# Kernel optimization log

Hardware: AMD Instinct MI355X
Metric: run time of the kernel (lower is better)

## Reference

```python
import jax, jax.numpy as jnp
import numpy as np

HIDDEN = 2048
NUM_HEADS = 16
HEAD_DIM = 128
BLOCK_SIZE = 64
NUM_ACTIVE_BLOCKS = 4  # diagonal pattern -> bandwidth = 2 blocks each side
NEG_INF = -1e30  # stand-in for -inf that is safe under softmax in fp32


def _block_diagonal_additive_mask(seq_len: int) -> jnp.ndarray:
    """Token-level additive mask [S, S]; 0 where block |bi-bj|<=bandwidth, -inf else."""
    bandwidth = NUM_ACTIVE_BLOCKS // 2
    bid = jnp.arange(seq_len) // BLOCK_SIZE  # [S]
    active = jnp.abs(bid[:, None] - bid[None, :]) <= bandwidth  # [S, S] bool
    return jnp.where(active, 0.0, NEG_INF).astype(jnp.float32)


def setup_inputs() -> dict:
    key = jax.random.key(0)
    k0, k1, k2, k3, k4 = jax.random.split(key, 5)
    B, S = 2, 2048
    scale = 1.0 / np.sqrt(HIDDEN)
    return {
        "hidden_states": jax.random.normal(k0, (B, S, HIDDEN), dtype=jnp.float32),
        "Wq": jax.random.normal(k1, (HIDDEN, NUM_HEADS * HEAD_DIM), dtype=jnp.float32) * scale,
        "Wk": jax.random.normal(k2, (HIDDEN, NUM_HEADS * HEAD_DIM), dtype=jnp.float32) * scale,
        "Wv": jax.random.normal(k3, (HIDDEN, NUM_HEADS * HEAD_DIM), dtype=jnp.float32) * scale,
        "Wo": jax.random.normal(k4, (NUM_HEADS * HEAD_DIM, HIDDEN), dtype=jnp.float32) * scale,
    }


def reference(hidden_states, Wq, Wk, Wv, Wo):
    B, S, _ = hidden_states.shape
    scaling = HEAD_DIM ** -0.5

    # projections -> [B, H, S, D]
    def split_heads(x):
        return x.reshape(B, S, NUM_HEADS, HEAD_DIM).transpose(0, 2, 1, 3)

    q = split_heads(hidden_states @ Wq)
    k = split_heads(hidden_states @ Wk)
    v = split_heads(hidden_states @ Wv)

    mask = _block_diagonal_additive_mask(S)  # [S, S]

    # scores [B, H, S, S]
    scores = jnp.einsum("bhsd,bhtd->bhst", q, k) * scaling + mask[None, None]
    attn = jax.nn.softmax(scores.astype(jnp.float32), axis=-1).astype(q.dtype)

    out = jnp.einsum("bhst,bhtd->bhsd", attn, v)  # [B, H, S, D]
    out = out.transpose(0, 2, 1, 3).reshape(B, S, NUM_HEADS * HEAD_DIM)
    return out @ Wo
```

## Files before the change

### kernel.cpp

```cpp
#include <hip/hip_runtime.h>

typedef __attribute__((ext_vector_type(4))) float f32x4;
typedef __attribute__((ext_vector_type(16))) float f32x16;
typedef __attribute__((ext_vector_type(8))) _Float16 f16x8;
typedef __attribute__((ext_vector_type(4))) _Float16 f16x4;

__device__ __forceinline__ void gload_lds16(const void* g, void* l) {
  __builtin_amdgcn_global_load_lds((__attribute__((address_space(1))) void*)(g),
                                   (__attribute__((address_space(3))) void*)(l), 16, 0, 0);
}

#define SB0() __builtin_amdgcn_sched_barrier(0)
#define WAITV6() asm volatile("s_waitcnt vmcnt(6)" ::: "memory")
#define WAITV0() asm volatile("s_waitcnt vmcnt(0)" ::: "memory")

__global__ __launch_bounds__(256) void prep(const float* __restrict__ Hs,
                                            const float* __restrict__ W0, const float* __restrict__ W1,
                                            const float* __restrict__ W2, const float* __restrict__ W3,
                                            _Float16* __restrict__ Hb, _Float16* __restrict__ Wt) {
  __shared__ _Float16 tile[64][65];
  const int bid = blockIdx.x, tid = threadIdx.x;
  if (bid < 8192) {
    int i = (bid * 256 + tid) * 4;
    float4 v = *(const float4*)(Hs + i);
    f16x4 o = { (_Float16)v.x, (_Float16)v.y, (_Float16)v.z, (_Float16)v.w };
    *(f16x4*)(Hb + i) = o;
    return;
  }
  const int t = bid - 8192;
  const int z = t >> 10, k0 = ((t >> 5) & 31) * 64, n0 = (t & 31) * 64;
  const float* W = z == 0 ? W0 : z == 1 ? W1 : z == 2 ? W2 : W3;
  _Float16* Wo_ = Wt + (size_t)z * (2048u * 2048u);
  #pragma unroll
  for (int p = 0; p < 4; ++p) {
    int o = p * 256 + tid, r = o >> 4, c = o & 15;
    float4 v = *(const float4*)(W + (size_t)(k0 + r) * 2048 + n0 + c * 4);
    tile[r][c * 4 + 0] = (_Float16)v.x;
    tile[r][c * 4 + 1] = (_Float16)v.y;
    tile[r][c * 4 + 2] = (_Float16)v.z;
    tile[r][c * 4 + 3] = (_Float16)v.w;
  }
  __syncthreads();
  #pragma unroll
  for (int p = 0; p < 2; ++p) {
    int o = p * 256 + tid, nl = o >> 3, c = o & 7;
    f16x8 u;
    #pragma unroll
    for (int i = 0; i < 8; ++i) u[i] = tile[c * 8 + i][nl];
    *(f16x8*)(Wo_ + (size_t)(n0 + nl) * 2048 + k0 + c * 8) = u;
  }
}

template <int SM, int SN, typename OutT>
__device__ __forceinline__ void gemm_tile(const _Float16* __restrict__ A,
                                          const _Float16* __restrict__ Bt,
                                          OutT* __restrict__ C,
                                          int K, int N, int m0, int n0, _Float16* S) {
  _Float16* As = S;
  _Float16* Bs = S + SM * 64 * 64;
  const int tid = threadIdx.x;
  const int lane = tid & 63, w = tid >> 6, l32 = lane & 31, half = lane >> 5;
  const int wm = (w & 1) * SM * 32, wn = (w >> 1) * SN * 32;
  f32x16 acc[SM][SN];
  #pragma unroll
  for (int s = 0; s < SM; ++s)
    #pragma unroll
    for (int t = 0; t < SN; ++t) acc[s][t] = 0;

  for (int k0 = 0; k0 < K; k0 += 64) {
    __syncthreads();
    #pragma unroll
    for (int p = 0; p < SM * 2; ++p) {
      int o = p * 256 + tid, r = o >> 3, c = o & 7;
      gload_lds16(A + (size_t)(m0 + r) * K + k0 + ((c ^ (r & 7)) * 8), (char*)As + o * 16);
    }
    #pragma unroll
    for (int p = 0; p < SN * 2; ++p) {
      int o = p * 256 + tid, r = o >> 3, c = o & 7;
      gload_lds16(Bt + (size_t)(n0 + r) * K + k0 + ((c ^ (r & 7)) * 8), (char*)Bs + o * 16);
    }
    __builtin_amdgcn_s_waitcnt(0);
    __syncthreads();
    #pragma unroll
    for (int kk = 0; kk < 4; ++kk) {
      const int slot = ((2 * kk + half) ^ (l32 & 7)) * 8;
      f16x8 af[SM], bf[SN];
      #pragma unroll
      for (int s = 0; s < SM; ++s) af[s] = *(const f16x8*)(As + (wm + s * 32 + l32) * 64 + slot);
      #pragma unroll
      for (int t = 0; t < SN; ++t) bf[t] = *(const f16x8*)(Bs + (wn + t * 32 + l32) * 64 + slot);
      #pragma unroll
      for (int s = 0; s < SM; ++s)
        #pragma unroll
        for (int t = 0; t < SN; ++t)
          acc[s][t] = __builtin_amdgcn_mfma_f32_32x32x16_f16(bf[t], af[s], acc[s][t], 0, 0, 0);
    }
  }
  #pragma unroll
  for (int s = 0; s < SM; ++s) {
    const size_t row = (size_t)(m0 + wm + s * 32 + l32);
    #pragma unroll
    for (int t = 0; t < SN; ++t) {
      #pragma unroll
      for (int g = 0; g < 4; ++g) {
        const int col = n0 + wn + t * 32 + g * 8 + 4 * half;
        if constexpr (sizeof(OutT) == 2) {
          f16x4 o = { (_Float16)acc[s][t][4 * g + 0], (_Float16)acc[s][t][4 * g + 1],
                      (_Float16)acc[s][t][4 * g + 2], (_Float16)acc[s][t][4 * g + 3] };
          *(f16x4*)((_Float16*)C + row * N + col) = o;
        } else {
          f32x4 o = { acc[s][t][4 * g + 0], acc[s][t][4 * g + 1],
                      acc[s][t][4 * g + 2], acc[s][t][4 * g + 3] };
          *(f32x4*)((float*)C + row * N + col) = o;
        }
      }
    }
  }
}

__device__ __forceinline__ void gemm256(const _Float16* __restrict__ A,
                                        const _Float16* __restrict__ Bt,
                                        _Float16* __restrict__ C, int ldc,
                                        int m0, int n0, _Float16* S) {
  _Float16* const As0 = S;
  _Float16* const As1 = S + 16384;
  _Float16* const Bs0 = S + 32768;
  _Float16* const Bs1 = S + 49152;
  const int tid = (int)threadIdx.x;
  const int lane = tid & 63, w = tid >> 6, l32 = lane & 31, half = lane >> 5;
  const int wm = (w & 1) * 128, wn = (w >> 1) * 64;

  f32x16 acc[4][2];
  #pragma unroll
  for (int s = 0; s < 4; ++s)
    #pragma unroll
    for (int t = 0; t < 2; ++t) acc[s][t] = 0;

  f16x8 af[2][4];
  f16x8 bf[2][4];

  auto stageA = [&](_Float16* dst, int ar, int kt) {
    const int r = tid >> 3, c = tid & 7;
    gload_lds16(A + (size_t)(m0 + ar + r) * 2048 + kt * 64 + ((c ^ (r & 7)) << 3),
                (char*)dst + ar * 128 + tid * 16);
  };
  auto stageB = [&](_Float16* dst, int br, int kt) {
    const int r = tid >> 3, c = tid & 7;
    gload_lds16(Bt + (size_t)(n0 + br + r) * 2048 + kt * 64 + ((c ^ (r & 7)) << 3),
                (char*)dst + br * 128 + tid * 16);
  };
  auto ldA = [&](const _Float16* as, int p) {
    #pragma unroll
    for (int s2 = 0; s2 < 2; ++s2)
      #pragma unroll
      for (int kk = 0; kk < 4; ++kk)
        af[s2][kk] = *(const f16x8*)(as + (wm + p * 64 + s2 * 32 + l32) * 64 +
                                     (((2 * kk + half) ^ (l32 & 7)) << 3));
  };
  auto ldB = [&](const _Float16* bs, int q) {
    #pragma unroll
    for (int kk = 0; kk < 4; ++kk)
      bf[q][kk] = *(const f16x8*)(bs + (wn + q * 32 + l32) * 64 +
                                  (((2 * kk + half) ^ (l32 & 7)) << 3));
  };
  auto mm = [&](int sp, int q) {
    __builtin_amdgcn_s_setprio(1);
    #pragma unroll
    for (int kk = 0; kk < 4; ++kk)
      #pragma unroll
      for (int s2 = 0; s2 < 2; ++s2)
        acc[sp * 2 + s2][q] = __builtin_amdgcn_mfma_f32_32x32x16_f16(
            bf[q][kk], af[s2][kk], acc[sp * 2 + s2][q], 0, 0, 0);
    __builtin_amdgcn_s_setprio(0);
  };

  auto tile = [&](int kt, _Float16* Ac, _Float16* Bc, _Float16* An, _Float16* Bn) {
    const bool g1 = (kt + 1) < 32, g2 = (kt + 2) < 32;
    ldA(Ac, 0); ldB(Bc, 0);
    if (g1) { stageA(An, 64, kt + 1); stageA(An, 192, kt + 1); }
    SB0(); __builtin_amdgcn_s_barrier(); SB0();
    mm(0, 0);
    SB0(); __builtin_amdgcn_s_barrier(); SB0();
    ldB(Bc, 1);
    if (g2) { stageA(Ac, 0, kt + 2); stageA(Ac, 128, kt + 2); }
    SB0(); __builtin_amdgcn_s_barrier(); SB0();
    mm(0, 1);
    SB0(); __builtin_amdgcn_s_barrier(); SB0();
    ldA(Ac, 1);
    if (g2) { stageB(Bc, 0, kt + 2); stageB(Bc, 64, kt + 2); }
    SB0(); __builtin_amdgcn_s_barrier(); SB0();
    mm(1, 1);
    SB0(); __builtin_amdgcn_s_barrier(); SB0();
    if (g2) { stageB(Bc, 128, kt + 2); stageB(Bc, 192, kt + 2); }
    if (g2) { WAITV6(); } else { WAITV0(); }
    SB0(); __builtin_amdgcn_s_barrier(); SB0();
    mm(1, 0);
    SB0(); __builtin_amdgcn_s_barrier(); SB0();
  };

  stageA(As0, 0, 0); stageA(As0, 64, 0); stageA(As0, 128, 0); stageA(As0, 192, 0);
  stageB(Bs0, 0, 0); stageB(Bs0, 64, 0); stageB(Bs0, 128, 0); stageB(Bs0, 192, 0);
  stageA(As1, 0, 1); stageA(As1, 128, 1);
  stageB(Bs1, 0, 1); stageB(Bs1, 64, 1); stageB(Bs1, 128, 1); stageB(Bs1, 192, 1);
  WAITV6();
  SB0(); __builtin_amdgcn_s_barrier(); SB0();

  #pragma unroll 1
  for (int kt = 0; kt < 32; kt += 2) {
    tile(kt, As0, Bs0, As1, Bs1);
    tile(kt + 1, As1, Bs1, As0, Bs0);
  }

  #pragma unroll
  for (int s = 0; s < 4; ++s) {
    const size_t row = (size_t)(wm + s * 32 + l32);
    #pragma unroll
    for (int t = 0; t < 2; ++t)
      #pragma unroll
      for (int g = 0; g < 4; ++g) {
        const int col = wn + t * 32 + g * 8 + 4 * half;
        f16x4 o = { (_Float16)acc[s][t][4 * g + 0], (_Float16)acc[s][t][4 * g + 1],
                    (_Float16)acc[s][t][4 * g + 2], (_Float16)acc[s][t][4 * g + 3] };
        *(f16x4*)(C + row * ldc + col) = o;
      }
  }
}

__global__ __launch_bounds__(512, 2) void qkvv8(const _Float16* __restrict__ Hb,
                                                const _Float16* __restrict__ Wt,
                                                _Float16* __restrict__ Qb,
                                                _Float16* __restrict__ Kb,
                                                _Float16* __restrict__ Vtb) {
  __shared__ _Float16 S[65536];
  const int id = blockIdx.x;
  if (id < 256) {
    const int m0 = (id >> 4) * 256, n0 = (id & 15) * 256;
    _Float16* C = (n0 < 2048 ? Qb + n0 : Kb + (n0 - 2048)) + (size_t)m0 * 2048;
    gemm256(Hb, Wt, C, 2048, m0, n0, S);
  } else {
    const int t = id - 256;
    const int m0 = (t >> 4) * 256, n0 = (t & 15) * 256;
    gemm256(Wt + (size_t)2 * 4194304, Hb, Vtb + (size_t)m0 * 4096 + n0, 4096, m0, n0, S);
  }
}

__global__ __launch_bounds__(256) void gemm_wo(const _Float16* __restrict__ A,
                                               const _Float16* __restrict__ Bt,
                                               float* __restrict__ C) {
  __shared__ _Float16 S[16384];
  const int t = blockIdx.x;
  gemm_tile<2, 2>(A, Bt, C, 2048, 2048, (t >> 4) * 128, (t & 15) * 128, S);
}

__global__ __launch_bounds__(256) void attn(const _Float16* __restrict__ Qg,
                                            const _Float16* __restrict__ Kg,
                                            const _Float16* __restrict__ Vtg,
                                            _Float16* __restrict__ Og) {
  const int t = blockIdx.x, h = blockIdx.y, b = blockIdx.z;
  __shared__ _Float16 Qs[128 * 128];
  __shared__ _Float16 Ks[64 * 128];
  __shared__ _Float16 Vs[128 * 64];
  const int tid = threadIdx.x;
  const int lane = tid & 63, w = tid >> 6, l16 = lane & 15, quad = lane >> 4;
  const int qbw = 2 * t + (w >> 1);
  const char* QsB = (const char*)Qs;
  const char* KsB = (const char*)Ks;
  const char* VsB = (const char*)Vs;

  #pragma unroll
  for (int p = 0; p < 8; ++p) {
    int o = p * 256 + tid, r = o >> 4, c = o & 15;
    gload_lds16(Qg + (size_t)(b * 2048 + t * 128 + r) * 2048 + h * 128 + ((c ^ (r & 15)) * 8),
                (char*)Qs + o * 16);
  }
  __builtin_amdgcn_s_waitcnt(0);
  __syncthreads();
  f16x8 qf[2][4];
  #pragma unroll
  for (int qc = 0; qc < 2; ++qc)
    #pragma unroll
    for (int ks = 0; ks < 4; ++ks)
      qf[qc][ks] = *(const f16x8*)(QsB + (w * 32 + qc * 16 + l16) * 256 +
                                   (((ks * 4 + quad) ^ l16) * 16));

  const float scale = 0.08838834764831845f;
  float m_[2] = {-1e30f, -1e30f}, l_[2] = {0.f, 0.f};
  f32x4 oacc[8][2];
  #pragma unroll
  for (int dt = 0; dt < 8; ++dt)
    #pragma unroll
    for (int qc = 0; qc < 2; ++qc) oacc[dt][qc] = (f32x4){0.f, 0.f, 0.f, 0.f};

  for (int jj = 0; jj < 6; ++jj) {
    const int j = 2 * t - 2 + jj;
    const int jc = j < 0 ? 0 : (j > 31 ? 31 : j);
    __syncthreads();
    #pragma unroll
    for (int p = 0; p < 4; ++p) {
      int o = p * 256 + tid, r = o >> 4, c = o & 15;
      gload_lds16(Kg + (size_t)(b * 2048 + jc * 64 + r) * 2048 + h * 128 + ((c ^ (r & 15)) * 8),
                  (char*)Ks + o * 16);
    }
    #pragma unroll
    for (int p = 0; p < 4; ++p) {
      int o = p * 256 + tid, d = o >> 3, c = o & 7;
      gload_lds16(Vtg + (size_t)(h * 128 + d) * 4096 + b * 2048 + jc * 64 + ((c ^ (d & 7)) * 8),
                  (char*)Vs + o * 16);
    }
    __builtin_amdgcn_s_waitcnt(0);
    __syncthreads();

    const bool valid = (j >= 0) && (j <= 31) && (j >= qbw - 2) && (j <= qbw + 2);
    if (valid) {
      f32x4 sc[4][2];
      #pragma unroll
      for (int kt = 0; kt < 4; ++kt)
        #pragma unroll
        for (int qc = 0; qc < 2; ++qc) sc[kt][qc] = (f32x4){0.f, 0.f, 0.f, 0.f};
      #pragma unroll
      for (int kt = 0; kt < 4; ++kt)
        #pragma unroll
        for (int ks = 0; ks < 4; ++ks) {
          f16x8 kf = *(const f16x8*)(KsB + (kt * 16 + l16) * 256 + (((ks * 4 + quad) ^ l16) * 16));
          #pragma unroll
          for (int qc = 0; qc < 2; ++qc)
            sc[kt][qc] = __builtin_amdgcn_mfma_f32_16x16x32_f16(kf, qf[qc][ks], sc[kt][qc], 0, 0, 0);
        }
      #pragma unroll
      for (int qc = 0; qc < 2; ++qc) {
        float mj = -1e30f;
        #pragma unroll
        for (int kt = 0; kt < 4; ++kt)
          #pragma unroll
          for (int r = 0; r < 4; ++r) {
            float v = sc[kt][qc][r] * scale;
            sc[kt][qc][r] = v;
            mj = fmaxf(mj, v);
          }
        mj = fmaxf(mj, __shfl_xor(mj, 16));
        mj = fmaxf(mj, __shfl_xor(mj, 32));
        const float mn = fmaxf(m_[qc], mj);
        const float alpha = __expf(m_[qc] - mn);
        float s_ = 0.f;
        #pragma unroll
        for (int kt = 0; kt < 4; ++kt)
          #pragma unroll
          for (int r = 0; r < 4; ++r) {
            float p = __expf(sc[kt][qc][r] - mn);
            sc[kt][qc][r] = p;
            s_ += p;
          }
        s_ += __shfl_xor(s_, 16);
        s_ += __shfl_xor(s_, 32);
        l_[qc] = l_[qc] * alpha + s_;
        m_[qc] = mn;
        #pragma unroll
        for (int dt = 0; dt < 8; ++dt) oacc[dt][qc] *= alpha;
      }
      #pragma unroll
      for (int kt = 0; kt < 4; ++kt) {
        f16x4 pb[2];
        #pragma unroll
        for (int qc = 0; qc < 2; ++qc)
          pb[qc] = (f16x4){ (_Float16)sc[kt][qc][0], (_Float16)sc[kt][qc][1],
                            (_Float16)sc[kt][qc][2], (_Float16)sc[kt][qc][3] };
        #pragma unroll
        for (int dt = 0; dt < 8; ++dt) {
          f16x4 vv = *(const f16x4*)(VsB + (dt * 16 + l16) * 128 +
                                     (((2 * kt + (quad >> 1)) ^ (l16 & 7)) * 16) + (quad & 1) * 8);
          #pragma unroll
          for (int qc = 0; qc < 2; ++qc)
            oacc[dt][qc] = __builtin_amdgcn_mfma_f32_16x16x16f16(vv, pb[qc], oacc[dt][qc], 0, 0, 0);
        }
      }
    }
  }

  #pragma unroll
  for (int qc = 0; qc < 2; ++qc) {
    const float pinv = 1.0f / l_[qc];
    const size_t orow = (size_t)(b * 2048 + t * 128 + w * 32 + qc * 16 + l16);
    #pragma unroll
    for (int dt = 0; dt < 8; ++dt) {
      f16x4 ov = { (_Float16)(oacc[dt][qc][0] * pinv), (_Float16)(oacc[dt][qc][1] * pinv),
                   (_Float16)(oacc[dt][qc][2] * pinv), (_Float16)(oacc[dt][qc][3] * pinv) };
      *(f16x4*)(Og + orow * 2048 + h * 128 + dt * 16 + quad * 4) = ov;
    }
  }
}

extern "C" void kernel_launch(void* const* d_in, const int* in_sizes, int n_in,
                              void* d_out, int out_size, void* d_ws, size_t ws_size,
                              hipStream_t stream) {
  const float* Hs = (const float*)d_in[0];
  const float* Wq = (const float*)d_in[1];
  const float* Wk = (const float*)d_in[2];
  const float* Wv = (const float*)d_in[3];
  const float* Wo = (const float*)d_in[4];
  _Float16* Hb  = (_Float16*)d_ws;
  _Float16* Wt  = Hb  + 8388608;
  _Float16* Qb  = Wt  + 16777216;
  _Float16* Kb  = Qb  + 8388608;
  _Float16* Vtb = Kb  + 8388608;
  _Float16* Ob  = Vtb + 8388608;
  float* out = (float*)d_out;

  prep<<<12288, 256, 0, stream>>>(Hs, Wq, Wk, Wv, Wo, Hb, Wt);
  qkvv8<<<384, 512, 0, stream>>>(Hb, Wt, Qb, Kb, Vtb);
  attn<<<dim3(16, 16, 2), 256, 0, stream>>>(Qb, Kb, Vtb, Ob);
  gemm_wo<<<512, 256, 0, stream>>>(Ob, Wt + (size_t)3 * 4194304, out);
}
```

Baseline: 361.9 us.

## Merge V projection into QK blocks and loosen GEMM pipeline barriers

The QKV kernel drops from 384 blocks to 256. Each block now computes one 256x256 Q/K tile and then a 128x256 tile of the transposed V projection, using a new 128-row GEMM helper, so per-block work is balanced across the CUs. The 256-tile GEMM main loop is rescheduled with fewer workgroup barriers: sched_barrier fences are removed, both B fragments are loaded up front, and the last two MFMA groups run back to back. This leaves more scheduling freedom to the compiler and cuts sync stalls, but it risks LDS hazards if the new staging order is wrong. It also lowers occupancy to one block per CU for the fused work.

```diff
diff --git a/kernel.cpp b/kernel.cpp
--- a/kernel.cpp
+++ b/kernel.cpp
@@ -10,7 +10,7 @@
                                    (__attribute__((address_space(3))) void*)(l), 16, 0, 0);
 }
 
-#define SB0() __builtin_amdgcn_sched_barrier(0)
+#define BAR() asm volatile("s_barrier" ::: "memory")
 #define WAITV6() asm volatile("s_waitcnt vmcnt(6)" ::: "memory")
 #define WAITV0() asm volatile("s_waitcnt vmcnt(0)" ::: "memory")
 
@@ -163,7 +163,7 @@
       bf[q][kk] = *(const f16x8*)(bs + (wn + q * 32 + l32) * 64 +
                                   (((2 * kk + half) ^ (l32 & 7)) << 3));
   };
-  auto mm = [&](int sp, int q) {
+  auto mm8 = [&](int sp, int q) {
     __builtin_amdgcn_s_setprio(1);
     #pragma unroll
     for (int kk = 0; kk < 4; ++kk)
@@ -172,30 +172,6 @@
         acc[sp * 2 + s2][q] = __builtin_amdgcn_mfma_f32_32x32x16_f16(
             bf[q][kk], af[s2][kk], acc[sp * 2 + s2][q], 0, 0, 0);
     __builtin_amdgcn_s_setprio(0);
-  };
-
-  auto tile = [&](int kt, _Float16* Ac, _Float16* Bc, _Float16* An, _Float16* Bn) {
-    const bool g1 = (kt + 1) < 32, g2 = (kt + 2) < 32;
-    ldA(Ac, 0); ldB(Bc, 0);
-    if (g1) { stageA(An, 64, kt + 1); stageA(An, 192, kt + 1); }
-    SB0(); __builtin_amdgcn_s_barrier(); SB0();
-    mm(0, 0);
-    SB0(); __builtin_amdgcn_s_barrier(); SB0();
-    ldB(Bc, 1);
-    if (g2) { stageA(Ac, 0, kt + 2); stageA(Ac, 128, kt + 2); }
-    SB0(); __builtin_amdgcn_s_barrier(); SB0();
-    mm(0, 1);
-    SB0(); __builtin_amdgcn_s_barrier(); SB0();
-    ldA(Ac, 1);
-    if (g2) { stageB(Bc, 0, kt + 2); stageB(Bc, 64, kt + 2); }
-    SB0(); __builtin_amdgcn_s_barrier(); SB0();
-    mm(1, 1);
-    SB0(); __builtin_amdgcn_s_barrier(); SB0();
-    if (g2) { stageB(Bc, 128, kt + 2); stageB(Bc, 192, kt + 2); }
-    if (g2) { WAITV6(); } else { WAITV0(); }
-    SB0(); __builtin_amdgcn_s_barrier(); SB0();
-    mm(1, 0);
-    SB0(); __builtin_amdgcn_s_barrier(); SB0();
   };
 
   stageA(As0, 0, 0); stageA(As0, 64, 0); stageA(As0, 128, 0); stageA(As0, 192, 0);
@@ -203,12 +179,31 @@
   stageA(As1, 0, 1); stageA(As1, 128, 1);
   stageB(Bs1, 0, 1); stageB(Bs1, 64, 1); stageB(Bs1, 128, 1); stageB(Bs1, 192, 1);
   WAITV6();
-  SB0(); __builtin_amdgcn_s_barrier(); SB0();
+  BAR();
+
+  auto tile = [&](int kt, _Float16* Ac, _Float16* Bc, _Float16* An) {
+    const bool g1 = (kt + 1) < 32, g2 = (kt + 2) < 32;
+    ldA(Ac, 0);
+    ldB(Bc, 0); ldB(Bc, 1);
+    if (g1) { stageA(An, 64, kt + 1); stageA(An, 192, kt + 1); }
+    mm8(0, 0);
+    BAR();
+    if (g2) { stageA(Ac, 0, kt + 2); stageA(Ac, 128, kt + 2); }
+    mm8(0, 1);
+    BAR();
+    ldA(Ac, 1);
+    if (g2) { stageB(Bc, 0, kt + 2); stageB(Bc, 64, kt + 2);
+              stageB(Bc, 128, kt + 2); stageB(Bc, 192, kt + 2); }
+    mm8(1, 1);
+    mm8(1, 0);
+    if (g2) { WAITV6(); } else { WAITV0(); }
+    BAR();
+  };
 
   #pragma unroll 1
   for (int kt = 0; kt < 32; kt += 2) {
-    tile(kt, As0, Bs0, As1, Bs1);
-    tile(kt + 1, As1, Bs1, As0, Bs0);
+    tile(kt, As0, Bs0, As1);
+    tile(kt + 1, As1, Bs1, As0);
   }
 
   #pragma unroll
@@ -226,21 +221,122 @@
   }
 }
 
-__global__ __launch_bounds__(512, 2) void qkvv8(const _Float16* __restrict__ Hb,
+__device__ __forceinline__ void gemm128(const _Float16* __restrict__ A,
+                                        const _Float16* __restrict__ Bt,
+                                        _Float16* __restrict__ C, int ldc,
+                                        int m0, int n0, _Float16* S) {
+  _Float16* const As0 = S;
+  _Float16* const As1 = S + 8192;
+  _Float16* const Bs0 = S + 16384;
+  _Float16* const Bs1 = S + 32768;
+  const int tid = (int)threadIdx.x;
+  const int lane = tid & 63, w = tid >> 6, l32 = lane & 31, half = lane >> 5;
+  const int wm = (w & 1) * 64, wn = (w >> 1) * 64;
+
+  f32x16 acc[2][2];
+  #pragma unroll
+  for (int s = 0; s < 2; ++s)
+    #pragma unroll
+    for (int t = 0; t < 2; ++t) acc[s][t] = 0;
+
+  f16x8 af[2][4], bf[2][4];
+
+  auto stA = [&](_Float16* dst, int ar, int kt) {
+    const int r = tid >> 3, c = tid & 7;
+    gload_lds16(A + (size_t)(m0 + ar + r) * 2048 + kt * 64 + ((c ^ (r & 7)) << 3),
+                (char*)dst + ar * 128 + tid * 16);
+  };
+  auto stB = [&](_Float16* dst, int br, int kt) {
+    const int r = tid >> 3, c = tid & 7;
+    gload_lds16(Bt + (size_t)(n0 + br + r) * 2048 + kt * 64 + ((c ^ (r & 7)) << 3),
+                (char*)dst + br * 128 + tid * 16);
+  };
+  auto ldA_ = [&](const _Float16* as) {
+    #pragma unroll
+    for (int s2 = 0; s2 < 2; ++s2)
+      #pragma unroll
+      for (int kk = 0; kk < 4; ++kk)
+        af[s2][kk] = *(const f16x8*)(as + (wm + s2 * 32 + l32) * 64 +
+                                     (((2 * kk + half) ^ (l32 & 7)) << 3));
+  };
+  auto ldB_ = [&](const _Float16* bs, int q) {
+    #pragma unroll
+    for (int kk = 0; kk < 4; ++kk)
+      bf[q][kk] = *(const f16x8*)(bs + (wn + q * 32 + l32) * 64 +
+                                  (((2 * kk + half) ^ (l32 & 7)) << 3));
+  };
+  auto mmq = [&](int q) {
+    __builtin_amdgcn_s_setprio(1);
+    #pragma unroll
+    for (int kk = 0; kk < 4; ++kk)
+      #pragma unroll
+      for (int s2 = 0; s2 < 2; ++s2)
+        acc[s2][q] = __builtin_amdgcn_mfma_f32_32x32x16_f16(
+            bf[q][kk], af[s2][kk], acc[s2][q], 0, 0, 0);
+    __builtin_amdgcn_s_setprio(0);
+  };
+
+  stA(As0, 0, 0); stA(As0, 64, 0);
+  stB(Bs0, 0, 0); stB(Bs0, 64, 0); stB(Bs0, 128, 0); stB(Bs0, 192, 0);
+  stA(As1, 0, 1); stA(As1, 64, 1);
+  stB(Bs1, 0, 1); stB(Bs1, 64, 1); stB(Bs1, 128, 1); stB(Bs1, 192, 1);
+  WAITV6();
+  BAR();
+
+  auto tile = [&](int kt, _Float16* Ac, _Float16* Bc) {
+    const bool g2 = (kt + 2) < 32;
+    ldA_(Ac); ldB_(Bc, 0); ldB_(Bc, 1);
+    mmq(0);
+    mmq(1);
+    BAR();
+    if (g2) {
+      stA(Ac, 0, kt + 2); stA(Ac, 64, kt + 2);
+      stB(Bc, 0, kt + 2); stB(Bc, 64, kt + 2); stB(Bc, 128, kt + 2); stB(Bc, 192, kt + 2);
+      WAITV6();
+    } else {
+      WAITV0();
+    }
+    BAR();
+  };
+
+  #pragma unroll 1
+  for (int kt = 0; kt < 32; kt += 2) {
+    tile(kt, As0, Bs0);
+    tile(kt + 1, As1, Bs1);
+  }
+
+  #pragma unroll
+  for (int s = 0; s < 2; ++s) {
+    const size_t row = (size_t)(wm + s * 32 + l32);
+    #pragma unroll
+    for (int t = 0; t < 2; ++t)
+      #pragma unroll
+      for (int g = 0; g < 4; ++g) {
+        const int col = wn + t * 32 + g * 8 + 4 * half;
+        f16x4 o = { (_Float16)acc[s][t][4 * g + 0], (_Float16)acc[s][t][4 * g + 1],
+                    (_Float16)acc[s][t][4 * g + 2], (_Float16)acc[s][t][4 * g + 3] };
+        *(f16x4*)(C + row * ldc + col) = o;
+      }
+  }
+}
+
+__global__ __launch_bounds__(512, 2) void qkvv3(const _Float16* __restrict__ Hb,
                                                 const _Float16* __restrict__ Wt,
                                                 _Float16* __restrict__ Qb,
                                                 _Float16* __restrict__ Kb,
                                                 _Float16* __restrict__ Vtb) {
   __shared__ _Float16 S[65536];
   const int id = blockIdx.x;
-  if (id < 256) {
+  {
     const int m0 = (id >> 4) * 256, n0 = (id & 15) * 256;
-    _Float16* C = (n0 < 2048 ? Qb + n0 : Kb + (n0 - 2048)) + (size_t)m0 * 2048;
-    gemm256(Hb, Wt, C, 2048, m0, n0, S);
-  } else {
-    const int t = id - 256;
-    const int m0 = (t >> 4) * 256, n0 = (t & 15) * 256;
-    gemm256(Wt + (size_t)2 * 4194304, Hb, Vtb + (size_t)m0 * 4096 + n0, 4096, m0, n0, S);
+    _Float16* Cq = (n0 < 2048 ? Qb + n0 : Kb + (n0 - 2048)) + (size_t)m0 * 2048;
+    gemm256(Hb, Wt, Cq, 2048, m0, n0, S);
+  }
+  WAITV0();
+  BAR();
+  {
+    const int m0 = (id >> 4) * 128, n0 = (id & 15) * 256;
+    gemm128(Wt + (size_t)2 * 4194304, Hb, Vtb + (size_t)m0 * 4096 + n0, 4096, m0, n0, S);
   }
 }
 
@@ -406,7 +502,7 @@
   float* out = (float*)d_out;
 
   prep<<<12288, 256, 0, stream>>>(Hs, Wq, Wk, Wv, Wo, Hb, Wt);
-  qkvv8<<<384, 512, 0, stream>>>(Hb, Wt, Qb, Kb, Vtb);
+  qkvv3<<<256, 512, 0, stream>>>(Hb, Wt, Qb, Kb, Vtb);
   attn<<<dim3(16, 16, 2), 256, 0, stream>>>(Qb, Kb, Vtb, Ob);
   gemm_wo<<<512, 256, 0, stream>>>(Ob, Wt + (size_t)3 * 4194304, out);
 }
```

Measured after the change: 341.0 us. 5.8% less time.
